# Performance work log

Measured on AMD Instinct MI355X. Metric: run time of the kernel, lower is better.

The kernel has to match this reference:

```python
import jax, jax.numpy as jnp
import numpy as np

B, S, D, H = 4, 2048, 1024, 16
DK = D // H
THETA = 10000.0


def _rope(x, pos):
    # x: [..., s, d_k] interleaved-pair rotation (GPT-NeoX/torch-from-scratch style)
    half = DK // 2
    inv_freq = 1.0 / (THETA ** (jnp.arange(half, dtype=jnp.float32) * 2.0 / DK))
    ang = pos.astype(jnp.float32)[:, None] * inv_freq  # [s, half]
    cos, sin = jnp.cos(ang), jnp.sin(ang)
    x1, x2 = x[..., 0::2], x[..., 1::2]
    out = jnp.stack([x1 * cos - x2 * sin, x1 * sin + x2 * cos], axis=-1)
    return out.reshape(x.shape)


def setup_inputs() -> dict:
    key = jax.random.key(0)
    ks = jax.random.split(key, 5)
    w_scale = 1.0 / np.sqrt(D)
    return {
        "x": jax.random.normal(ks[0], (B, S, D), dtype=jnp.float32),
        "W_q": jax.random.normal(ks[1], (D, D), dtype=jnp.float32) * w_scale,
        "W_k": jax.random.normal(ks[2], (D, D), dtype=jnp.float32) * w_scale,
        "W_v": jax.random.normal(ks[3], (D, D), dtype=jnp.float32) * w_scale,
        "W_o": jax.random.normal(ks[4], (D, D), dtype=jnp.float32) * w_scale,
        "token_positions": jnp.arange(S, dtype=jnp.int32),
    }


def reference(x, W_q, W_k, W_v, W_o, token_positions):
    b, s, d = x.shape

    def proj(W):  # x @ W.T, split heads -> [b, h, s, d_k]
        y = jnp.einsum('bsd,ed->bse', x, W)
        return y.reshape(b, s, H, DK).transpose(0, 2, 1, 3)

    Q, K, V = proj(W_q), proj(W_k), proj(W_v)
    Q = _rope(Q, token_positions)
    K = _rope(K, token_positions)

    scores = jnp.einsum('bhqd,bhkd->bhqk', Q, K) / jnp.sqrt(jnp.float32(DK))
    causal = jnp.tril(jnp.ones((s, s), dtype=bool))
    scores = jnp.where(causal, scores, -jnp.inf)
    attn = jax.nn.softmax(scores, axis=-1)
    out = jnp.einsum('bhqk,bhkd->bhqd', attn, V)
    out = out.transpose(0, 2, 1, 3).reshape(b, s, d)
    return jnp.einsum('bsd,ed->bse', out, W_o)
```

## Files before the change

### kernel.cpp

```cpp
#include <hip/hip_runtime.h>
#include <stdint.h>

#define B_ 4
#define S_ 2048
#define D_ 1024
#define H_ 16
#define DK_ 64
#define M_ (B_*S_)

typedef __attribute__((ext_vector_type(8))) short short8;
typedef __attribute__((ext_vector_type(4))) float f32x4;
typedef __attribute__((ext_vector_type(16))) float f32x16;
typedef __attribute__((ext_vector_type(2))) unsigned int u32x2;

static __device__ __forceinline__ float bf2f(unsigned short s) {
  union { unsigned u; float f; } v; v.u = ((unsigned)s) << 16; return v.f;
}
static __device__ __forceinline__ unsigned short f2bf(float f) {
  union { float f; unsigned u; } v; v.f = f;
  unsigned r = v.u + 0x7fffu + ((v.u >> 16) & 1u);
  return (unsigned short)(r >> 16);
}
static __device__ __forceinline__ unsigned cvtpk_bf16(float lo, float hi) {
  unsigned r;
  asm("v_cvt_pk_bf16_f32 %0, %1, %2" : "=v"(r) : "v"(lo), "v"(hi));
  return r;
}

#define GLDS16(g, l) __builtin_amdgcn_global_load_lds( \
    (const __attribute__((address_space(1))) unsigned int*)(g), \
    (__attribute__((address_space(3))) unsigned int*)(l), 16, 0, 0)

__global__ void rope_tab_kernel(const int* __restrict__ pos, float2* __restrict__ tab) {
  int idx = blockIdx.x * 256 + threadIdx.x;
  int s = idx >> 5, j = idx & 31;
  float freq = exp2f(-(float)j * (13.287712379549449f / 32.0f));
  float ang = (float)pos[s] * freq;
  float sn, cs;
  sincosf(ang, &sn, &cs);
  tab[idx] = make_float2(cs, sn);
}

__global__ void cvt_all_kernel(const float* __restrict__ x,
                               const float* __restrict__ w0, const float* __restrict__ w1,
                               const float* __restrict__ w2, const float* __restrict__ w3,
                               unsigned short* __restrict__ xb,
                               unsigned short* __restrict__ o0, unsigned short* __restrict__ o1,
                               unsigned short* __restrict__ o2, unsigned short* __restrict__ o3) {
  int idx = blockIdx.x * 256 + threadIdx.x;
  const float* src; unsigned short* dst; int i;
  if (idx < 2097152) { src = x; dst = xb; i = idx; }
  else {
    int widx = idx - 2097152;
    int w = widx >> 18; i = widx & 262143;
    src = (w == 0) ? w0 : (w == 1) ? w1 : (w == 2) ? w2 : w3;
    dst = (w == 0) ? o0 : (w == 1) ? o1 : (w == 2) ? o2 : o3;
  }
  float4 v = ((const float4*)src)[i];
  ushort4 o;
  o.x = f2bf(v.x); o.y = f2bf(v.y); o.z = f2bf(v.z); o.w = f2bf(v.w);
  ((ushort4*)dst)[i] = o;
}

#define GEMM_BODY \
  __shared__ __align__(16) char lA[2][128*128]; \
  __shared__ __align__(16) char lB[2][128*128]; \
  int t = threadIdx.x; \
  int wave = t >> 6, lane = t & 63; \
  int ln15 = lane & 15, lgrp = lane >> 4; \
  int wr = wave >> 1, wc = wave & 1; \
  f32x4 acc[4][4]; \
  _Pragma("unroll") \
  for (int m = 0; m < 4; ++m) \
    _Pragma("unroll") \
    for (int n = 0; n < 4; ++n) { f32x4 z = {0.f,0.f,0.f,0.f}; acc[m][n] = z; } \
  const char* pA[4]; const char* pB[4]; int sdst[4]; \
  _Pragma("unroll") \
  for (int i_ = 0; i_ < 4; ++i_) { \
    int a_ = (i_*256 + t) << 4; \
    int r_ = a_ >> 7; \
    int cb_ = (a_ & 127) ^ ((r_ & 7) << 4); \
    sdst[i_] = a_; \
    pA[i_] = Ab + (size_t)r_*(K*2) + cb_; \
    pB[i_] = Bb + (size_t)r_*(K*2) + cb_; \
  } \
  GSTAGE(0); \
  __syncthreads(); \
  { int cur = 0; \
    for (int k0 = 0; k0 < K; k0 += 64) { \
      if (k0 + 64 < K) GSTAGE(cur ^ 1); \
      GEMM_COMPUTE(cur); \
      __syncthreads(); \
      cur ^= 1; \
    } }

#define GSTAGE(bufi) do { \
    _Pragma("unroll") \
    for (int i_ = 0; i_ < 4; ++i_) { \
      GLDS16(pA[i_], lA[bufi] + sdst[i_]); \
      GLDS16(pB[i_], lB[bufi] + sdst[i_]); \
      pA[i_] += 128; pB[i_] += 128; \
    } \
  } while (0)

#define GEMM_COMPUTE(bufi) do { \
    const char* cA_ = lA[bufi]; \
    const char* cB_ = lB[bufi]; \
    _Pragma("unroll") \
    for (int kf = 0; kf < 2; ++kf) { \
      int cb = kf*64 + lgrp*16; \
      short8 af[4], bfr[4]; \
      _Pragma("unroll") \
      for (int m = 0; m < 4; ++m) { \
        int r = wr*64 + m*16 + ln15; \
        af[m] = *(const short8*)(cA_ + r*128 + (cb ^ ((r & 7) << 4))); \
      } \
      _Pragma("unroll") \
      for (int n = 0; n < 4; ++n) { \
        int r = wc*64 + n*16 + ln15; \
        bfr[n] = *(const short8*)(cB_ + r*128 + (cb ^ ((r & 7) << 4))); \
      } \
      __builtin_amdgcn_s_setprio(1); \
      _Pragma("unroll") \
      for (int m = 0; m < 4; ++m) \
        _Pragma("unroll") \
        for (int n = 0; n < 4; ++n) \
          acc[m][n] = __builtin_amdgcn_mfma_f32_16x16x32_bf16(af[m], bfr[n], acc[m][n], 0, 0, 0); \
      __builtin_amdgcn_s_setprio(0); \
    } \
  } while (0)

__global__ __launch_bounds__(256) void gemm_qk(const unsigned short* __restrict__ A,
                                               const unsigned short* __restrict__ W,
                                               const float2* __restrict__ Tab,
                                               unsigned short* __restrict__ Qo,
                                               unsigned short* __restrict__ Ko) {
  const int K = 1024;
  int bn = blockIdx.x;
  int bm = blockIdx.y;
  const char* Ab = (const char*)A + (size_t)bm * 128 * (K*2);
  const char* Bb = (const char*)W + (size_t)bn * 128 * (K*2);
  GEMM_BODY

  unsigned short* Out = (bn < 8) ? Qo : Ko;
  float qs = (bn < 8) ? (0.125f * 1.4426950408889634f) : 1.0f;
#pragma unroll
  for (int m = 0; m < 4; ++m)
#pragma unroll
    for (int n = 0; n < 4; ++n)
#pragma unroll
      for (int r = 0; r < 4; ++r) {
        int row = bm*128 + wr*64 + m*16 + lgrp*4 + r;
        int cc = (bn & 7)*128 + wc*64 + n*16 + ln15;
        int b = row >> 11, s = row & (S_-1);
        int h = cc >> 6, dk = cc & 63;
        float v = acc[m][n][r];
        float p = __shfl_xor(v, 1);
        float2 cssn = Tab[(s << 5) + (dk >> 1)];
        float sgn = (dk & 1) ? cssn.y : -cssn.y;
        float o = (v * cssn.x + p * sgn) * qs;
        Out[(((size_t)(b*H_ + h)*S_ + s) << 6) + dk] = f2bf(o);
      }
}

__global__ __launch_bounds__(256) void gemm_v(const unsigned short* __restrict__ A,
                                              const unsigned short* __restrict__ W,
                                              unsigned short* __restrict__ Vo) {
  const int K = 1024;
  int bx = blockIdx.x;
  int bm = bx >> 3, bn = bx & 7;
  const char* Ab = (const char*)A + (size_t)bm * 128 * (K*2);
  const char* Bb = (const char*)W + (size_t)bn * 128 * (K*2);
  GEMM_BODY

#pragma unroll
  for (int m = 0; m < 4; ++m)
#pragma unroll
    for (int n = 0; n < 4; ++n)
#pragma unroll
      for (int r = 0; r < 4; ++r) {
        int row = bm*128 + wr*64 + m*16 + lgrp*4 + r;
        int cc = bn*128 + wc*64 + n*16 + ln15;
        int b = row >> 11, s = row & (S_-1);
        int h = cc >> 6, dk = cc & 63;
        Vo[(((size_t)(b*H_ + h)*DK_ + dk) * S_) + s] = f2bf(acc[m][n][r]);
      }
}

__global__ __launch_bounds__(256) void gemm_out(const unsigned short* __restrict__ A,
                                                const unsigned short* __restrict__ W,
                                                float* __restrict__ Out) {
  const int K = 1024, N = 1024;
  int bx = blockIdx.x;
  int bm = bx >> 3, bn = bx & 7;
  const char* Ab = (const char*)A + (size_t)bm * 128 * (K*2);
  const char* Bb = (const char*)W + (size_t)bn * 128 * (K*2);
  GEMM_BODY

#pragma unroll
  for (int m = 0; m < 4; ++m)
#pragma unroll
    for (int n = 0; n < 4; ++n)
#pragma unroll
      for (int r = 0; r < 4; ++r) {
        int row = bm*128 + wr*64 + m*16 + lgrp*4 + r;
        int col = bn*128 + wc*64 + n*16 + ln15;
        Out[(size_t)row * N + col] = acc[m][n][r];
      }
}

__global__ __launch_bounds__(256) void attn_kernel(const unsigned short* __restrict__ Q,
                                                   const unsigned short* __restrict__ Kg,
                                                   const unsigned short* __restrict__ VT,
                                                   unsigned short* __restrict__ O) {
  int bid = blockIdx.x;
  int bh = bid & 63;
  int qt = 15 - (bid >> 6);
  int b = bh >> 4, h = bh & 15;
  const int qbase = qt * 128;
  const unsigned short* Qp = Q + (((size_t)bh * S_ + qbase) << 6);
  const char* Kp = (const char*)(Kg + ((size_t)bh * S_ << 6));
  const char* Vp = (const char*)(VT + (size_t)bh * DK_ * S_);

  __shared__ __align__(16) char lK[3][64*128];
  __shared__ __align__(16) char lV[3][64*128];

  int t = threadIdx.x, wave = t >> 6, lane = t & 63;
  int ln31 = lane & 31, hi = lane >> 5;
  int qw = wave * 32;
  int qg = qbase + qw + ln31;

  short8 qf[4];
#pragma unroll
  for (int kk = 0; kk < 4; ++kk)
    qf[kk] = *(const short8*)(Qp + (size_t)(qw + ln31)*64 + kk*16 + hi*8);

  f32x16 oc[2];
#pragma unroll
  for (int dh = 0; dh < 2; ++dh)
#pragma unroll
    for (int r = 0; r < 16; ++r) oc[dh][r] = 0.f;
  float li = 0.f;

  const int nt = 2*qt + 2;

  const char* pK[2]; const char* pV[2]; int kdst[2];
#pragma unroll
  for (int i_ = 0; i_ < 2; ++i_) {
    int a_ = ((i_*256 + t) << 4);
    int r_ = a_ >> 7;
    int cb_ = (a_ & 127) ^ ((r_ & 7) << 4);
    kdst[i_] = a_;
    pK[i_] = Kp + (size_t)r_*128 + cb_;
    pV[i_] = Vp + (size_t)r_*(S_*2) + cb_;
  }
#define STAGE_KV(kbuf, vbuf) do { \
    _Pragma("unroll") \
    for (int i_ = 0; i_ < 2; ++i_) { \
      GLDS16(pK[i_], (kbuf) + kdst[i_]); \
      GLDS16(pV[i_], (vbuf) + kdst[i_]); \
      pK[i_] += 64*128; pV[i_] += 128; \
    } \
  } while (0)

  char *Ka = lK[0], *Kb_ = lK[1], *Kc = lK[2];
  char *Va = lV[0], *Vb = lV[1], *Vc = lV[2];

  STAGE_KV(Ka, Va);
  STAGE_KV(Kb_, Vb);
  asm volatile("s_waitcnt vmcnt(4)" ::: "memory");
  __builtin_amdgcn_s_barrier();

  for (int kt = 0; kt < nt; ++kt) {
    bool more = (kt + 2 < nt);
    if (more) STAGE_KV(Kc, Vc);

    const char* cK = Ka;
    const char* cV = Va;
    bool active = (kt*64 <= qbase + qw + 31);
    bool diag   = (kt*64 + 63 > qbase + qw);

    if (active) {
      f32x16 sc[2];
      __builtin_amdgcn_s_setprio(1);
#pragma unroll
      for (int t2 = 0; t2 < 2; ++t2) {
        f32x16 a;
#pragma unroll
        for (int r = 0; r < 16; ++r) a[r] = 0.f;
        int rK = t2*32 + ln31;
        int swz = (rK & 7) << 4;
#pragma unroll
        for (int kk = 0; kk < 4; ++kk) {
          short8 kfr = *(const short8*)(cK + rK*128 + ((kk*32 + hi*16) ^ swz));
          a = __builtin_amdgcn_mfma_f32_32x32x16_bf16(kfr, qf[kk], a, 0, 0, 0);
        }
        sc[t2] = a;
      }
      __builtin_amdgcn_s_setprio(0);

      if (diag) {
#pragma unroll
        for (int t2 = 0; t2 < 2; ++t2)
#pragma unroll
          for (int r = 0; r < 16; ++r) {
            int kv = kt*64 + t2*32 + (r & 3) + 8*(r >> 2) + 4*hi;
            if (kv > qg) sc[t2][r] = -__builtin_inff();
          }
      }

      float lss[4] = {0.f, 0.f, 0.f, 0.f};
#pragma unroll
      for (int t2 = 0; t2 < 2; ++t2)
#pragma unroll
        for (int r = 0; r < 16; ++r) {
          float pv = __builtin_amdgcn_exp2f(sc[t2][r]);
          sc[t2][r] = pv; lss[r & 3] += pv;
        }
      li += (lss[0] + lss[1]) + (lss[2] + lss[3]);

#pragma unroll
      for (int kk = 0; kk < 4; ++kk) {
        int base = 8*(kk & 1), tt = kk >> 1;
        unsigned P0 = cvtpk_bf16(sc[tt][base+0], sc[tt][base+1]);
        unsigned P1 = cvtpk_bf16(sc[tt][base+2], sc[tt][base+3]);
        unsigned Q0 = cvtpk_bf16(sc[tt][base+4], sc[tt][base+5]);
        unsigned Q1 = cvtpk_bf16(sc[tt][base+6], sc[tt][base+7]);
        u32x2 r01 = __builtin_amdgcn_permlane32_swap(P0, Q0, false, false);
        u32x2 s01 = __builtin_amdgcn_permlane32_swap(P1, Q1, false, false);
        union { unsigned u[4]; short8 s8; } pf;
        pf.u[0] = r01[0]; pf.u[1] = s01[0]; pf.u[2] = r01[1]; pf.u[3] = s01[1];
        __builtin_amdgcn_s_setprio(1);
#pragma unroll
        for (int dh = 0; dh < 2; ++dh) {
          int rV = dh*32 + ln31;
          short8 vfr = *(const short8*)(cV + rV*128 + (((kk*32 + hi*16)) ^ ((rV & 7) << 4)));
          oc[dh] = __builtin_amdgcn_mfma_f32_32x32x16_bf16(vfr, pf.s8, oc[dh], 0, 0, 0);
        }
        __builtin_amdgcn_s_setprio(0);
      }
    }

    if (more) asm volatile("s_waitcnt vmcnt(4)" ::: "memory");
    else      asm volatile("s_waitcnt vmcnt(0)" ::: "memory");
    __builtin_amdgcn_s_barrier();

    char* tk = Ka; Ka = Kb_; Kb_ = Kc; Kc = tk;
    char* tv = Va; Va = Vb;  Vb = Vc;  Vc = tv;
  }
#undef STAGE_KV

  float lf = li + __shfl_xor(li, 32);
  float rinv = 1.0f / lf;
#pragma unroll
  for (int dh = 0; dh < 2; ++dh)
#pragma unroll
    for (int rg = 0; rg < 4; ++rg) {
      ushort4 pk4;
      pk4.x = f2bf(oc[dh][rg*4+0] * rinv);
      pk4.y = f2bf(oc[dh][rg*4+1] * rinv);
      pk4.z = f2bf(oc[dh][rg*4+2] * rinv);
      pk4.w = f2bf(oc[dh][rg*4+3] * rinv);
      int dk = dh*32 + 8*rg + 4*hi;
      *(ushort4*)(O + (((size_t)(b*S_ + qg)) << 10) + h*64 + dk) = pk4;
    }
}

extern "C" void kernel_launch(void* const* d_in, const int* in_sizes, int n_in,
                              void* d_out, int out_size, void* d_ws, size_t ws_size,
                              hipStream_t stream) {
  const float* x  = (const float*)d_in[0];
  const float* Wq = (const float*)d_in[1];
  const float* Wk = (const float*)d_in[2];
  const float* Wv = (const float*)d_in[3];
  const float* Wo = (const float*)d_in[4];
  const int* pos  = (const int*)d_in[5];

  char* ws = (char*)d_ws;
  unsigned short* xb  = (unsigned short*)(ws + 0);
  unsigned short* wqb = (unsigned short*)(ws + 16777216);
  unsigned short* wkb = (unsigned short*)(ws + 18874368);
  unsigned short* wvb = (unsigned short*)(ws + 20971520);
  unsigned short* wob = (unsigned short*)(ws + 23068672);
  unsigned short* Qb  = (unsigned short*)(ws + 25165824);
  unsigned short* Kb  = (unsigned short*)(ws + 41943040);
  unsigned short* VTb = (unsigned short*)(ws + 58720256);
  float2* tab = (float2*)VTb;
  unsigned short* Ob  = xb;

  rope_tab_kernel<<<256, 256, 0, stream>>>(pos, tab);
  cvt_all_kernel<<<12288, 256, 0, stream>>>(x, Wq, Wk, Wv, Wo, xb, wqb, wkb, wvb, wob);

  gemm_qk<<<dim3(16, 64), 256, 0, stream>>>(xb, wqb, tab, Qb, Kb);
  gemm_v<<<512, 256, 0, stream>>>(xb, wvb, VTb);

  attn_kernel<<<1024, 256, 0, stream>>>(Qb, Kb, VTb, Ob);

  gemm_out<<<512, 256, 0, stream>>>(Ob, wob, (float*)d_out);
}
```

Measured before the change: 167.9 us.

## Switch GEMM mainloop to triple-buffered K=32 stages with vmcnt waits

The projection GEMM mainloop moves from a double-buffered K=64 stage with __syncthreads to a three-stage ring of K=32 tiles. Two tiles stay in flight, and waits are explicit s_waitcnt vmcnt plus raw barriers. The LDS layout is repacked so two 64-byte rows share one 128-byte swizzled line. The goal is to hide global-load latency better while keeping LDS use lower, at the cost of more barriers per K and hand-tuned waitcnt counts that must match the load count exactly.

```diff
diff --git a/kernel.cpp b/kernel.cpp
--- a/kernel.cpp
+++ b/kernel.cpp
@@ -63,8 +63,8 @@
 }
 
 #define GEMM_BODY \
-  __shared__ __align__(16) char lA[2][128*128]; \
-  __shared__ __align__(16) char lB[2][128*128]; \
+  __shared__ __align__(16) char lA[3][8192]; \
+  __shared__ __align__(16) char lB[3][8192]; \
   int t = threadIdx.x; \
   int wave = t >> 6, lane = t & 63; \
   int ln15 = lane & 15, lgrp = lane >> 4; \
@@ -74,60 +74,66 @@
   for (int m = 0; m < 4; ++m) \
     _Pragma("unroll") \
     for (int n = 0; n < 4; ++n) { f32x4 z = {0.f,0.f,0.f,0.f}; acc[m][n] = z; } \
-  const char* pA[4]; const char* pB[4]; int sdst[4]; \
+  const char* pA[2]; const char* pB[2]; int sdst[2]; \
   _Pragma("unroll") \
-  for (int i_ = 0; i_ < 4; ++i_) { \
-    int a_ = (i_*256 + t) << 4; \
-    int r_ = a_ >> 7; \
-    int cb_ = (a_ & 127) ^ ((r_ & 7) << 4); \
-    sdst[i_] = a_; \
-    pA[i_] = Ab + (size_t)r_*(K*2) + cb_; \
-    pB[i_] = Bb + (size_t)r_*(K*2) + cb_; \
+  for (int c_ = 0; c_ < 2; ++c_) { \
+    int a_ = (c_*256 + t) << 4;                  \
+    int R_ = a_ >> 7; \
+    int u_ = (a_ & 127) ^ ((R_ & 7) << 4); \
+    int r_ = 2*R_ + (u_ >> 6);                   \
+    int cb_ = u_ & 63; \
+    sdst[c_] = a_; \
+    pA[c_] = Ab + (size_t)r_*(K*2) + cb_; \
+    pB[c_] = Bb + (size_t)r_*(K*2) + cb_; \
   } \
-  GSTAGE(0); \
-  __syncthreads(); \
+  GSTAGE3(0); \
+  GSTAGE3(1); \
+  asm volatile("s_waitcnt vmcnt(4)" ::: "memory"); \
+  __builtin_amdgcn_s_barrier(); \
   { int cur = 0; \
-    for (int k0 = 0; k0 < K; k0 += 64) { \
-      if (k0 + 64 < K) GSTAGE(cur ^ 1); \
-      GEMM_COMPUTE(cur); \
-      __syncthreads(); \
-      cur ^= 1; \
+    for (int kt = 0; kt < 32; ++kt) { \
+      bool more = (kt + 2 < 32); \
+      if (more) GSTAGE3((cur + 2) % 3); \
+      GCOMP3(cur); \
+      if (more) asm volatile("s_waitcnt vmcnt(4)" ::: "memory"); \
+      else      asm volatile("s_waitcnt vmcnt(0)" ::: "memory"); \
+      __builtin_amdgcn_s_barrier(); \
+      cur = (cur + 1) % 3; \
     } }
 
-#define GSTAGE(bufi) do { \
-    _Pragma("unroll") \
-    for (int i_ = 0; i_ < 4; ++i_) { \
-      GLDS16(pA[i_], lA[bufi] + sdst[i_]); \
-      GLDS16(pB[i_], lB[bufi] + sdst[i_]); \
-      pA[i_] += 128; pB[i_] += 128; \
+#define GSTAGE3(bufi) do { \
+    _Pragma("unroll") \
+    for (int c_ = 0; c_ < 2; ++c_) { \
+      GLDS16(pA[c_], lA[bufi] + sdst[c_]); \
+      GLDS16(pB[c_], lB[bufi] + sdst[c_]); \
+      pA[c_] += 64; pB[c_] += 64;              \
     } \
   } while (0)
 
-#define GEMM_COMPUTE(bufi) do { \
+#define GCOMP3(bufi) do { \
     const char* cA_ = lA[bufi]; \
     const char* cB_ = lB[bufi]; \
-    _Pragma("unroll") \
-    for (int kf = 0; kf < 2; ++kf) { \
-      int cb = kf*64 + lgrp*16; \
-      short8 af[4], bfr[4]; \
+    int cb = lgrp*16; \
+    short8 af[4], bfr[4]; \
+    _Pragma("unroll") \
+    for (int m = 0; m < 4; ++m) { \
+      int r = wr*64 + m*16 + ln15; \
+      int R = r >> 1; \
+      af[m] = *(const short8*)(cA_ + R*128 + (((((r & 1) << 6) | cb)) ^ ((R & 7) << 4))); \
+    } \
+    _Pragma("unroll") \
+    for (int n = 0; n < 4; ++n) { \
+      int r = wc*64 + n*16 + ln15; \
+      int R = r >> 1; \
+      bfr[n] = *(const short8*)(cB_ + R*128 + (((((r & 1) << 6) | cb)) ^ ((R & 7) << 4))); \
+    } \
+    __builtin_amdgcn_s_setprio(1); \
+    _Pragma("unroll") \
+    for (int m = 0; m < 4; ++m) \
       _Pragma("unroll") \
-      for (int m = 0; m < 4; ++m) { \
-        int r = wr*64 + m*16 + ln15; \
-        af[m] = *(const short8*)(cA_ + r*128 + (cb ^ ((r & 7) << 4))); \
-      } \
-      _Pragma("unroll") \
-      for (int n = 0; n < 4; ++n) { \
-        int r = wc*64 + n*16 + ln15; \
-        bfr[n] = *(const short8*)(cB_ + r*128 + (cb ^ ((r & 7) << 4))); \
-      } \
-      __builtin_amdgcn_s_setprio(1); \
-      _Pragma("unroll") \
-      for (int m = 0; m < 4; ++m) \
-        _Pragma("unroll") \
-        for (int n = 0; n < 4; ++n) \
-          acc[m][n] = __builtin_amdgcn_mfma_f32_16x16x32_bf16(af[m], bfr[n], acc[m][n], 0, 0, 0); \
-      __builtin_amdgcn_s_setprio(0); \
-    } \
+      for (int n = 0; n < 4; ++n) \
+        acc[m][n] = __builtin_amdgcn_mfma_f32_16x16x32_bf16(af[m], bfr[n], acc[m][n], 0, 0, 0); \
+    __builtin_amdgcn_s_setprio(0); \
   } while (0)
 
 __global__ __launch_bounds__(256) void gemm_qk(const unsigned short* __restrict__ A,
```

After: 188.4 us. 1.12x slower.
